# Kernel tuning notes

Measured on AMD Instinct MI355X. Metric: run time of the kernel, lower is better.

Reference implementation:

```python
import jax, jax.numpy as jnp
import numpy as np

T, B, D_IN, D_H, D_OUT, N_LAYERS = 512, 64, 512, 1024, 512, 2
LN_EPS = 1e-5


def _gru_layer(x_seq, h0, w_ih, w_hh, b_ih, b_hh):
    # x_seq: [T,B,D_in], h0: [B,H]; w_ih: [3H,D_in], w_hh: [3H,H]
    # Precompute input-side gate projections for all timesteps at once.
    xg = jnp.einsum('tbd,gd->tbg', x_seq, w_ih) + b_ih  # [T,B,3H]

    def step(h, xg_t):
        hg = h @ w_hh.T + b_hh                         # [B,3H]
        xr, xz, xn = jnp.split(xg_t, 3, axis=-1)
        hr, hz, hn = jnp.split(hg, 3, axis=-1)
        r = jax.nn.sigmoid(xr + hr)
        z = jax.nn.sigmoid(xz + hz)
        n = jnp.tanh(xn + r * hn)
        h_new = (1.0 - z) * n + z * h
        return h_new, h_new

    _, ys = jax.lax.scan(step, h0, xg)                 # ys: [T,B,H]
    return ys


def setup_inputs() -> dict:
    key = jax.random.key(0)
    ks = jax.random.split(key, 16)
    s_in = 1.0 / np.sqrt(D_H)
    inp = {
        'x': jax.random.normal(ks[0], (T, B, D_IN), dtype=jnp.float32),
        'h': jax.random.normal(ks[1], (N_LAYERS, B, D_H), dtype=jnp.float32),
        # GRU layer 0 (input dim D_IN)
        'w_ih0': jax.random.uniform(ks[2], (3 * D_H, D_IN), minval=-s_in, maxval=s_in),
        'w_hh0': jax.random.uniform(ks[3], (3 * D_H, D_H), minval=-s_in, maxval=s_in),
        'b_ih0': jax.random.uniform(ks[4], (3 * D_H,), minval=-s_in, maxval=s_in),
        'b_hh0': jax.random.uniform(ks[5], (3 * D_H,), minval=-s_in, maxval=s_in),
        # GRU layer 1 (input dim D_H)
        'w_ih1': jax.random.uniform(ks[6], (3 * D_H, D_H), minval=-s_in, maxval=s_in),
        'w_hh1': jax.random.uniform(ks[7], (3 * D_H, D_H), minval=-s_in, maxval=s_in),
        'b_ih1': jax.random.uniform(ks[8], (3 * D_H,), minval=-s_in, maxval=s_in),
        'b_hh1': jax.random.uniform(ks[9], (3 * D_H,), minval=-s_in, maxval=s_in),
        # LayerNorm
        'ln_gamma': jnp.ones((D_H,), dtype=jnp.float32),
        'ln_beta': jnp.zeros((D_H,), dtype=jnp.float32),
        # Output linear
        'ff_w': jax.random.uniform(ks[10], (D_OUT, D_H), minval=-s_in, maxval=s_in),
        'ff_b': jax.random.uniform(ks[11], (D_OUT,), minval=-s_in, maxval=s_in),
    }
    return inp


def reference(x, h, w_ih0, w_hh0, b_ih0, b_hh0, w_ih1, w_hh1, b_ih1, b_hh1,
              ln_gamma, ln_beta, ff_w, ff_b):
    y0 = _gru_layer(x, h[0], w_ih0, w_hh0, b_ih0, b_hh0)   # [T,B,H]
    y1 = _gru_layer(y0, h[1], w_ih1, w_hh1, b_ih1, b_hh1)  # [T,B,H]
    # LayerNorm over last dim
    mu = jnp.mean(y1, axis=-1, keepdims=True)
    var = jnp.mean(jnp.square(y1 - mu), axis=-1, keepdims=True)
    yn = (y1 - mu) * jax.lax.rsqrt(var + LN_EPS) * ln_gamma + ln_beta
    # Output projection
    out = jnp.einsum('tbh,oh->tbo', yn, ff_w) + ff_b       # [T,B,D_OUT]
    return out
```

## Files before the change

kernel.cpp:

```cpp
#include <hip/hip_runtime.h>

#define T_SEQ 512
#define BATCH 64
#define DIN0  512
#define D_H   1024
#define D_OUT 512
#define NBLK  256

typedef __attribute__((ext_vector_type(8))) short short8;
typedef __attribute__((ext_vector_type(4))) float f32x4;

__device__ inline float bf2f(unsigned short u) {
    unsigned x = ((unsigned)u) << 16;
    return __builtin_bit_cast(float, x);
}
__device__ inline unsigned short f2bf(float f) {
    unsigned x = __builtin_bit_cast(unsigned, f);
    unsigned r = (x + 0x7fffu + ((x >> 16) & 1u)) >> 16;
    return (unsigned short)r;
}
__device__ inline float fast_sigmoid(float x) { return 1.f / (1.f + __expf(-x)); }
__device__ inline float fast_tanh(float x) {
    float ax = fabsf(x);
    float t = __expf(-2.f * ax);
    float r = (1.f - t) / (1.f + t);
    return copysignf(r, x);
}

__device__ inline void store_u16_sc01(void* p, unsigned v) {
    asm volatile("global_store_short %0, %1, off sc0 sc1" :: "v"(p), "v"(v) : "memory");
}
__device__ inline void store_flag(int* p, int v) {
    asm volatile("global_store_dword %0, %1, off sc0 sc1" :: "v"(p), "v"(v) : "memory");
}
__device__ inline int load_flag(const int* p) {
    int r;
    asm volatile("global_load_dword %0, %1, off sc0 sc1\n\ts_waitcnt vmcnt(0)"
                 : "=&v"(r) : "v"(p) : "memory");
    return r;
}
__device__ inline short8 load16_sc01(const void* p) {
    short8 r;
    asm volatile("global_load_dwordx4 %0, %1, off sc0 sc1"
                 : "=&v"(r) : "v"(p) : "memory");
    return r;
}

__global__ void cast_kernel(const float* __restrict__ in, unsigned short* __restrict__ out, int n4) {
    int i = blockIdx.x * blockDim.x + threadIdx.x;
    int stride = gridDim.x * blockDim.x;
    for (; i < n4; i += stride) {
        float4 v = ((const float4*)in)[i];
        ushort4 o;
        o.x = f2bf(v.x); o.y = f2bf(v.y); o.z = f2bf(v.z); o.w = f2bf(v.w);
        ((ushort4*)out)[i] = o;
    }
}

template <int DIN, bool FULLZ>
__global__ __launch_bounds__(64, 1) void gru_scan(
    const unsigned short* __restrict__ xseq,
    const unsigned short* __restrict__ wih,
    const unsigned short* __restrict__ whh,
    const float* __restrict__ bih, const float* __restrict__ bhh,
    const float* __restrict__ h0,
    unsigned short* __restrict__ hbuf,
    unsigned short* __restrict__ Y,
    int* __restrict__ flags)
{
    extern __shared__ unsigned short lds[];
    constexpr int KT = D_H + DIN;

    const int lane = threadIdx.x;
    const int bid  = blockIdx.x;
    const int xcd = bid & 7;
    const int rg  = xcd >> 1;
    const int cb  = ((bid >> 3) << 1) | (xcd & 1);
    const int c0  = cb * 16, r0 = rg * 16;

    int* const frg   = flags + rg * 1024;
    int* const myflg = frg + cb * 16;

    const int NG = FULLZ ? 3 : 2;
    for (int g = 0; g < NG; ++g) {
        const int grow = (g == 0) ? 2 * D_H : (g == 1 ? 0 : D_H);
        unsigned short* W = lds + g * 16 * KT;
        for (int i = lane; i < 16 * (D_H / 8); i += 64) {
            int c = i >> 7, kb = i & 127;
            int el = (c * KT + kb * 8) ^ ((c & 7) << 3);
            *(short8*)&W[el] = *(const short8*)&whh[(size_t)(grow + c0 + c) * D_H + kb * 8];
        }
        for (int i = lane; i < 16 * (DIN / 8); i += 64) {
            int c = i / (DIN / 8), kb = i % (DIN / 8);
            int el = (c * KT + D_H + kb * 8) ^ ((c & 7) << 3);
            *(short8*)&W[el] = *(const short8*)&wih[(size_t)(grow + c0 + c) * DIN + kb * 8];
        }
    }
    if (!FULLZ) {
        for (int i = lane; i < 16 * (D_H / 8); i += 64) {
            int c = i >> 7, kb = i & 127;
            int el = 32 * KT + ((c * D_H + kb * 8) ^ ((c & 7) << 3));
            *(short8*)&lds[el] = *(const short8*)&whh[(size_t)(D_H + c0 + c) * D_H + kb * 8];
        }
    }
    __syncthreads();

    const int gc   = c0 + (lane & 15);
    const int crow = (lane >> 4) * 4;
    float hprev[4];
    #pragma unroll
    for (int i = 0; i < 4; ++i) {
        float v = h0[(size_t)(r0 + crow + i) * D_H + gc];
        hprev[i] = v;
        store_u16_sc01(&hbuf[(size_t)(r0 + crow + i) * D_H + gc], (unsigned)f2bf(v));
    }
    asm volatile("s_waitcnt vmcnt(0)" ::: "memory");
    if (lane == 0) store_flag(myflg, 1);

    const float b_r  = bih[gc] + bhh[gc];
    const float b_z  = bih[D_H + gc] + bhh[D_H + gc];
    const float b_xn = bih[2 * D_H + gc];
    const float b_hn = bhh[2 * D_H + gc];

    const int arow = lane & 15;
    const int ako  = (lane >> 4) * 8;
    const int swz  = (arow & 7) << 3;

    for (int t = 0; t < T_SEQ; ++t) {
        const unsigned short* hb  = hbuf + (t & 1) * (BATCH * D_H);
        unsigned short*       hbn = hbuf + ((t & 1) ^ 1) * (BATCH * D_H);
        const unsigned short* xt  = xseq + (size_t)t * BATCH * DIN;
        unsigned short*       Yt  = Y + (size_t)t * BATCH * D_H;

        f32x4 fr = {0.f, 0.f, 0.f, 0.f}, fz = fr, fnx = fr, fnh = fr;

        #pragma unroll 4
        for (int k = 0; k < DIN; k += 32) {
            short8 a  = *(const short8*)&xt[(size_t)(r0 + arow) * DIN + k + ako];
            int el    = (arow * KT + D_H + k + ako) ^ swz;
            short8 bn = *(const short8*)&lds[el];
            short8 br = *(const short8*)&lds[16 * KT + el];
            short8 bz;
            if (FULLZ) bz = *(const short8*)&lds[32 * KT + el];
            else       bz = *(const short8*)&wih[(size_t)(D_H + c0 + arow) * DIN + k + ako];
            fr  = __builtin_amdgcn_mfma_f32_16x16x32_bf16(a, br, fr, 0, 0, 0);
            fz  = __builtin_amdgcn_mfma_f32_16x16x32_bf16(a, bz, fz, 0, 0, 0);
            fnx = __builtin_amdgcn_mfma_f32_16x16x32_bf16(a, bn, fnx, 0, 0, 0);
        }

        {
            const int p = t + 1;
            const int* fp = frg + lane * 16;
            while (true) {
                int f = load_flag(fp);
                if (__all(f >= p)) break;
            }
        }

        short8 hfrag[32];
        const unsigned short* hrow = hb + (size_t)(r0 + arow) * D_H + ako;
        #pragma unroll
        for (int kk = 0; kk < 32; ++kk)
            hfrag[kk] = load16_sc01(hrow + kk * 32);
        asm volatile("s_waitcnt vmcnt(0)" ::: "memory");
        __builtin_amdgcn_sched_barrier(0);

        #pragma unroll
        for (int kk = 0; kk < 32; ++kk) {
            const int k = kk * 32;
            int el    = (arow * KT + k + ako) ^ swz;
            short8 bn = *(const short8*)&lds[el];
            short8 br = *(const short8*)&lds[16 * KT + el];
            int zel   = FULLZ ? (32 * KT + el)
                              : (32 * KT + ((arow * D_H + k + ako) ^ swz));
            short8 bz = *(const short8*)&lds[zel];
            fr  = __builtin_amdgcn_mfma_f32_16x16x32_bf16(hfrag[kk], br, fr, 0, 0, 0);
            fz  = __builtin_amdgcn_mfma_f32_16x16x32_bf16(hfrag[kk], bz, fz, 0, 0, 0);
            fnh = __builtin_amdgcn_mfma_f32_16x16x32_bf16(hfrag[kk], bn, fnh, 0, 0, 0);
        }

        #pragma unroll
        for (int i = 0; i < 4; ++i) {
            int rr = r0 + crow + i;
            float r = fast_sigmoid(fr[i] + b_r);
            float z = fast_sigmoid(fz[i] + b_z);
            float n = fast_tanh(fnx[i] + b_xn + r * (fnh[i] + b_hn));
            float hn = (1.f - z) * n + z * hprev[i];
            hprev[i] = hn;
            unsigned short h16 = f2bf(hn);
            store_u16_sc01(&hbn[(size_t)rr * D_H + gc], (unsigned)h16);
            Yt[(size_t)rr * D_H + gc] = h16;
        }
        asm volatile("s_waitcnt vmcnt(0)" ::: "memory");
        if (lane == 0) store_flag(myflg, t + 2);
    }
}

__global__ __launch_bounds__(256) void ln_proj(
    const unsigned short* __restrict__ y1,
    const float* __restrict__ gamma, const float* __restrict__ beta,
    const unsigned short* __restrict__ ffw,
    const float* __restrict__ ffb,
    float* __restrict__ out)
{
    __shared__ unsigned short ylds[16 * 1024];
    const int row0 = blockIdx.x * 16;
    const int tid = threadIdx.x;

    {
        const int rr = tid >> 4, l16 = tid & 15;
        const unsigned short* yrow = y1 + (size_t)(row0 + rr) * D_H;
        float s = 0.f, sq = 0.f;
        #pragma unroll
        for (int j8 = 0; j8 < 8; ++j8) {
            int k = l16 * 64 + j8 * 8;
            short8 v = *(const short8*)&yrow[k];
            int idx = (rr * 1024 + k) ^ ((rr & 7) << 3);
            *(short8*)&ylds[idx] = v;
            #pragma unroll
            for (int j = 0; j < 8; ++j) {
                float f = bf2f((unsigned short)v[j]);
                s += f; sq += f * f;
            }
        }
        #pragma unroll
        for (int o = 1; o < 16; o <<= 1) {
            s  += __shfl_xor(s, o, 64);
            sq += __shfl_xor(sq, o, 64);
        }
        float mu = s * (1.f / 1024.f);
        float var = sq * (1.f / 1024.f) - mu * mu;
        float rstd = rsqrtf(var + 1e-5f);
        #pragma unroll
        for (int j8 = 0; j8 < 8; ++j8) {
            int k = l16 * 64 + j8 * 8;
            int idx = (rr * 1024 + k) ^ ((rr & 7) << 3);
            short8 v = *(short8*)&ylds[idx];
            short8 o8;
            #pragma unroll
            for (int j = 0; j < 8; ++j) {
                float f = bf2f((unsigned short)v[j]);
                f = (f - mu) * rstd * gamma[k + j] + beta[k + j];
                o8[j] = (short)f2bf(f);
            }
            *(short8*)&ylds[idx] = o8;
        }
    }
    __syncthreads();

    const int w = tid >> 6, lane = tid & 63;
    const int cbase = w * 128;
    const int arow = lane & 15, ako = (lane >> 4) * 8;
    f32x4 acc[8] = {};
    for (int k = 0; k < D_H; k += 32) {
        int aidx = (arow * 1024 + k + ako) ^ ((arow & 7) << 3);
        short8 a = *(const short8*)&ylds[aidx];
        #pragma unroll
        for (int n = 0; n < 8; ++n) {
            int col = cbase + n * 16 + (lane & 15);
            short8 b = *(const short8*)&ffw[col * 1024 + k + ako];
            acc[n] = __builtin_amdgcn_mfma_f32_16x16x32_bf16(a, b, acc[n], 0, 0, 0);
        }
    }
    #pragma unroll
    for (int n = 0; n < 8; ++n) {
        int col = cbase + n * 16 + (lane & 15);
        float bb = ffb[col];
        #pragma unroll
        for (int i = 0; i < 4; ++i) {
            int rr = row0 + (lane >> 4) * 4 + i;
            out[(size_t)rr * D_OUT + col] = acc[n][i] + bb;
        }
    }
}

extern "C" void kernel_launch(void* const* d_in, const int* in_sizes, int n_in,
                              void* d_out, int out_size, void* d_ws, size_t ws_size,
                              hipStream_t stream) {
    const float* x     = (const float*)d_in[0];
    const float* h     = (const float*)d_in[1];
    const float* w_ih0 = (const float*)d_in[2];
    const float* w_hh0 = (const float*)d_in[3];
    const float* b_ih0 = (const float*)d_in[4];
    const float* b_hh0 = (const float*)d_in[5];
    const float* w_ih1 = (const float*)d_in[6];
    const float* w_hh1 = (const float*)d_in[7];
    const float* b_ih1 = (const float*)d_in[8];
    const float* b_hh1 = (const float*)d_in[9];
    const float* ln_g  = (const float*)d_in[10];
    const float* ln_b  = (const float*)d_in[11];
    const float* ff_w  = (const float*)d_in[12];
    const float* ff_b  = (const float*)d_in[13];
    float* out = (float*)d_out;

    char* ws = (char*)d_ws;
    size_t off = 0;
    auto alloc = [&](size_t bytes) {
        void* p = ws + off;
        off = (off + bytes + 255) & ~(size_t)255;
        return p;
    };
    unsigned short* x_bf   = (unsigned short*)alloc((size_t)T_SEQ * BATCH * DIN0 * 2);
    unsigned short* y1_bf  = (unsigned short*)alloc((size_t)T_SEQ * BATCH * D_H * 2);
    unsigned short* wih0_b = (unsigned short*)alloc((size_t)3 * D_H * DIN0 * 2);
    unsigned short* whh0_b = (unsigned short*)alloc((size_t)3 * D_H * D_H * 2);
    unsigned short* wih1_b = (unsigned short*)alloc((size_t)3 * D_H * D_H * 2);
    unsigned short* whh1_b = (unsigned short*)alloc((size_t)3 * D_H * D_H * 2);
    unsigned short* ffw_b  = (unsigned short*)alloc((size_t)D_OUT * D_H * 2);
    unsigned short* hbuf   = (unsigned short*)alloc((size_t)2 * BATCH * D_H * 2);
    int*            flags  = (int*)alloc(2 * 4096 * 4);
    if (off > ws_size) return;

    unsigned short* y0_bf = (unsigned short*)d_out;

    hipMemsetAsync(flags, 0, 2 * 4096 * 4, stream);

    auto castl = [&](const float* src, unsigned short* dst, int n) {
        int n4 = n / 4;
        int blocks = (n4 + 255) / 256;
        if (blocks > 2048) blocks = 2048;
        hipLaunchKernelGGL(cast_kernel, dim3(blocks), dim3(256), 0, stream, src, dst, n4);
    };
    castl(x,     x_bf,   T_SEQ * BATCH * DIN0);
    castl(w_ih0, wih0_b, 3 * D_H * DIN0);
    castl(w_hh0, whh0_b, 3 * D_H * D_H);
    castl(w_ih1, wih1_b, 3 * D_H * D_H);
    castl(w_hh1, whh1_b, 3 * D_H * D_H);
    castl(ff_w,  ffw_b,  D_OUT * D_H);

    const int lds0 = 48 * (D_H + DIN0) * 2;
    const int lds1 = 32 * (D_H + D_H) * 2 + 16 * D_H * 2;
    hipFuncSetAttribute((const void*)&gru_scan<DIN0, true>,
                        hipFuncAttributeMaxDynamicSharedMemorySize, lds0);
    hipFuncSetAttribute((const void*)&gru_scan<D_H, false>,
                        hipFuncAttributeMaxDynamicSharedMemorySize, lds1);

    hipLaunchKernelGGL((gru_scan<DIN0, true>), dim3(NBLK), dim3(64), lds0, stream,
        x_bf, wih0_b, whh0_b, b_ih0, b_hh0, h, hbuf, y0_bf, flags);
    hipLaunchKernelGGL((gru_scan<D_H, false>), dim3(NBLK), dim3(64), lds1, stream,
        y0_bf, wih1_b, whh1_b, b_ih1, b_hh1, h + BATCH * D_H, hbuf, y1_bf,
        flags + 4096);
    hipLaunchKernelGGL(ln_proj, dim3(T_SEQ * BATCH / 16), dim3(256), 0, stream,
        y1_bf, ln_g, ln_b, ffw_b, ff_b, out);
}
```

Baseline: 8.312 ms.

## Tile hidden-state buffer and chunk flag waits to overlap recurrent matmul with sync

Changes the hidden-state exchange buffer to a tiled 16x16 layout and packs per-block progress flags as 16-bit values so one 16-byte load checks eight producers. The recurrent matmul is split into eight chunks, each waiting only on the eight blocks that produce that slice of h, so MFMA work can start before all 64 producers finish. The Y store moves after the flag publish, and the spin loop gains s_sleep and an iteration cap. The cap risks silently proceeding with stale data on a timeout, and the many small waits add latency.

```diff
diff --git a/kernel.cpp b/kernel.cpp
--- a/kernel.cpp
+++ b/kernel.cpp
@@ -6,6 +6,7 @@
 #define D_H   1024
 #define D_OUT 512
 #define NBLK  256
+#define TILES 65536
 
 typedef __attribute__((ext_vector_type(8))) short short8;
 typedef __attribute__((ext_vector_type(4))) float f32x4;
@@ -30,21 +31,20 @@
 __device__ inline void store_u16_sc01(void* p, unsigned v) {
     asm volatile("global_store_short %0, %1, off sc0 sc1" :: "v"(p), "v"(v) : "memory");
 }
-__device__ inline void store_flag(int* p, int v) {
-    asm volatile("global_store_dword %0, %1, off sc0 sc1" :: "v"(p), "v"(v) : "memory");
-}
-__device__ inline int load_flag(const int* p) {
-    int r;
-    asm volatile("global_load_dword %0, %1, off sc0 sc1\n\ts_waitcnt vmcnt(0)"
-                 : "=&v"(r) : "v"(p) : "memory");
-    return r;
-}
 __device__ inline short8 load16_sc01(const void* p) {
     short8 r;
     asm volatile("global_load_dwordx4 %0, %1, off sc0 sc1"
                  : "=&v"(r) : "v"(p) : "memory");
     return r;
 }
+__device__ inline short8 load16_sc01_wait(const void* p) {
+    short8 r;
+    asm volatile("global_load_dwordx4 %0, %1, off sc0 sc1\n\ts_waitcnt vmcnt(0)"
+                 : "=&v"(r) : "v"(p) : "memory");
+    return r;
+}
+
+#define MFMA16(a, b, c) __builtin_amdgcn_mfma_f32_16x16x32_bf16((a), (b), (c), 0, 0, 0)
 
 __global__ void cast_kernel(const float* __restrict__ in, unsigned short* __restrict__ out, int n4) {
     int i = blockIdx.x * blockDim.x + threadIdx.x;
@@ -66,133 +66,141 @@
     const float* __restrict__ h0,
     unsigned short* __restrict__ hbuf,
     unsigned short* __restrict__ Y,
-    int* __restrict__ flags)
+    unsigned short* __restrict__ flags)
 {
     extern __shared__ unsigned short lds[];
-    constexpr int KT = D_H + DIN;
+    constexpr int KT = 1024 + DIN;
 
     const int lane = threadIdx.x;
     const int bid  = blockIdx.x;
-    const int xcd = bid & 7;
-    const int rg  = xcd >> 1;
-    const int cb  = ((bid >> 3) << 1) | (xcd & 1);
-    const int c0  = cb * 16, r0 = rg * 16;
-
-    int* const frg   = flags + rg * 1024;
-    int* const myflg = frg + cb * 16;
+    const int xcd  = bid & 7;
+    const int rg   = xcd >> 1;
+    const int cb   = ((bid >> 3) << 1) | (xcd & 1);
+    const int c0   = cb * 16, r0 = rg * 16;
+    const int tile = rg * 64 + cb;
+
+    unsigned short* const frg   = flags + rg * 64;
+    unsigned short* const myflg = frg + cb;
 
     const int NG = FULLZ ? 3 : 2;
     for (int g = 0; g < NG; ++g) {
         const int grow = (g == 0) ? 2 * D_H : (g == 1 ? 0 : D_H);
         unsigned short* W = lds + g * 16 * KT;
-        for (int i = lane; i < 16 * (D_H / 8); i += 64) {
+        for (int i = lane; i < 16 * 128; i += 64) {
             int c = i >> 7, kb = i & 127;
             int el = (c * KT + kb * 8) ^ ((c & 7) << 3);
             *(short8*)&W[el] = *(const short8*)&whh[(size_t)(grow + c0 + c) * D_H + kb * 8];
         }
         for (int i = lane; i < 16 * (DIN / 8); i += 64) {
             int c = i / (DIN / 8), kb = i % (DIN / 8);
-            int el = (c * KT + D_H + kb * 8) ^ ((c & 7) << 3);
+            int el = (c * KT + 1024 + kb * 8) ^ ((c & 7) << 3);
             *(short8*)&W[el] = *(const short8*)&wih[(size_t)(grow + c0 + c) * DIN + kb * 8];
         }
     }
     if (!FULLZ) {
-        for (int i = lane; i < 16 * (D_H / 8); i += 64) {
+        for (int i = lane; i < 16 * 128; i += 64) {
             int c = i >> 7, kb = i & 127;
-            int el = 32 * KT + ((c * D_H + kb * 8) ^ ((c & 7) << 3));
+            int el = 32 * KT + ((c * 1024 + kb * 8) ^ ((c & 7) << 3));
             *(short8*)&lds[el] = *(const short8*)&whh[(size_t)(D_H + c0 + c) * D_H + kb * 8];
         }
     }
-    __syncthreads();
-
-    const int gc   = c0 + (lane & 15);
+
+    const int arow = lane & 15;
+    const int ako  = (lane >> 4) * 8;
+    const int swz  = (arow & 7) << 3;
+    const int gc   = c0 + arow;
     const int crow = (lane >> 4) * 4;
+
+    const float b_r  = bih[gc] + bhh[gc];
+    const float b_z  = bih[D_H + gc] + bhh[D_H + gc];
+    const float b_xn = bih[2 * D_H + gc];
+    const float b_hn = bhh[2 * D_H + gc];
+
     float hprev[4];
     #pragma unroll
     for (int i = 0; i < 4; ++i) {
         float v = h0[(size_t)(r0 + crow + i) * D_H + gc];
         hprev[i] = v;
-        store_u16_sc01(&hbuf[(size_t)(r0 + crow + i) * D_H + gc], (unsigned)f2bf(v));
+        store_u16_sc01(&hbuf[tile * 256 + (crow + i) * 16 + arow], (unsigned)f2bf(v));
     }
     asm volatile("s_waitcnt vmcnt(0)" ::: "memory");
-    if (lane == 0) store_flag(myflg, 1);
-
-    const float b_r  = bih[gc] + bhh[gc];
-    const float b_z  = bih[D_H + gc] + bhh[D_H + gc];
-    const float b_xn = bih[2 * D_H + gc];
-    const float b_hn = bhh[2 * D_H + gc];
-
-    const int arow = lane & 15;
-    const int ako  = (lane >> 4) * 8;
-    const int swz  = (arow & 7) << 3;
+    if (lane == 0) store_u16_sc01(myflg, 1u);
 
     for (int t = 0; t < T_SEQ; ++t) {
-        const unsigned short* hb  = hbuf + (t & 1) * (BATCH * D_H);
-        unsigned short*       hbn = hbuf + ((t & 1) ^ 1) * (BATCH * D_H);
+        const unsigned short* hb  = hbuf + (t & 1) * TILES;
+        unsigned short*       hbn = hbuf + ((t & 1) ^ 1) * TILES;
         const unsigned short* xt  = xseq + (size_t)t * BATCH * DIN;
         unsigned short*       Yt  = Y + (size_t)t * BATCH * D_H;
 
-        f32x4 fr = {0.f, 0.f, 0.f, 0.f}, fz = fr, fnx = fr, fnh = fr;
+        f32x4 fr = {0.f,0.f,0.f,0.f}, fz = fr, fnx = fr, fnh = fr;
 
         #pragma unroll 4
         for (int k = 0; k < DIN; k += 32) {
             short8 a  = *(const short8*)&xt[(size_t)(r0 + arow) * DIN + k + ako];
-            int el    = (arow * KT + D_H + k + ako) ^ swz;
+            int el    = (arow * KT + 1024 + k + ako) ^ swz;
             short8 bn = *(const short8*)&lds[el];
             short8 br = *(const short8*)&lds[16 * KT + el];
             short8 bz;
             if (FULLZ) bz = *(const short8*)&lds[32 * KT + el];
             else       bz = *(const short8*)&wih[(size_t)(D_H + c0 + arow) * DIN + k + ako];
-            fr  = __builtin_amdgcn_mfma_f32_16x16x32_bf16(a, br, fr, 0, 0, 0);
-            fz  = __builtin_amdgcn_mfma_f32_16x16x32_bf16(a, bz, fz, 0, 0, 0);
-            fnx = __builtin_amdgcn_mfma_f32_16x16x32_bf16(a, bn, fnx, 0, 0, 0);
-        }
-
-        {
-            const int p = t + 1;
-            const int* fp = frg + lane * 16;
-            while (true) {
-                int f = load_flag(fp);
-                if (__all(f >= p)) break;
-            }
-        }
-
-        short8 hfrag[32];
-        const unsigned short* hrow = hb + (size_t)(r0 + arow) * D_H + ako;
-        #pragma unroll
-        for (int kk = 0; kk < 32; ++kk)
-            hfrag[kk] = load16_sc01(hrow + kk * 32);
-        asm volatile("s_waitcnt vmcnt(0)" ::: "memory");
-        __builtin_amdgcn_sched_barrier(0);
-
-        #pragma unroll
-        for (int kk = 0; kk < 32; ++kk) {
-            const int k = kk * 32;
-            int el    = (arow * KT + k + ako) ^ swz;
-            short8 bn = *(const short8*)&lds[el];
-            short8 br = *(const short8*)&lds[16 * KT + el];
-            int zel   = FULLZ ? (32 * KT + el)
-                              : (32 * KT + ((arow * D_H + k + ako) ^ swz));
-            short8 bz = *(const short8*)&lds[zel];
-            fr  = __builtin_amdgcn_mfma_f32_16x16x32_bf16(hfrag[kk], br, fr, 0, 0, 0);
-            fz  = __builtin_amdgcn_mfma_f32_16x16x32_bf16(hfrag[kk], bz, fz, 0, 0, 0);
-            fnh = __builtin_amdgcn_mfma_f32_16x16x32_bf16(hfrag[kk], bn, fnh, 0, 0, 0);
-        }
-
+            fnx = MFMA16(a, bn, fnx);
+            fr  = MFMA16(a, br, fr);
+            fz  = MFMA16(a, bz, fz);
+        }
+
+        for (int c = 0; c < 8; ++c) {
+            const int ch = (c + (cb & 7)) & 7;
+            {
+                const unsigned short* fp = frg + ch * 8;
+                for (int it = 0; it < 100000; ++it) {
+                    short8 f = load16_sc01_wait(fp);
+                    bool ok = true;
+                    #pragma unroll
+                    for (int j = 0; j < 8; ++j)
+                        ok &= ((unsigned short)f[j] >= (unsigned)(t + 1));
+                    if (__all(ok)) break;
+                    __builtin_amdgcn_s_sleep(1);
+                }
+            }
+            short8 hf[4];
+            #pragma unroll
+            for (int m = 0; m < 4; ++m) {
+                int tk = rg * 64 + ch * 8 + m * 2 + (ako >> 4);
+                hf[m] = load16_sc01(hb + (size_t)tk * 256 + arow * 16 + (ako & 8));
+            }
+            asm volatile("s_waitcnt vmcnt(0)" ::: "memory");
+            __builtin_amdgcn_sched_barrier(0);
+            #pragma unroll
+            for (int m = 0; m < 4; ++m) {
+                const int k = ch * 128 + m * 32;
+                int el    = (arow * KT + k + ako) ^ swz;
+                short8 bn = *(const short8*)&lds[el];
+                short8 br = *(const short8*)&lds[16 * KT + el];
+                short8 bz;
+                if (FULLZ) bz = *(const short8*)&lds[32 * KT + el];
+                else       bz = *(const short8*)&lds[32 * KT + ((arow * 1024 + k + ako) ^ swz)];
+                fnh = MFMA16(hf[m], bn, fnh);
+                fr  = MFMA16(hf[m], br, fr);
+                fz  = MFMA16(hf[m], bz, fz);
+            }
+        }
+
+        unsigned short h16[4];
         #pragma unroll
         for (int i = 0; i < 4; ++i) {
-            int rr = r0 + crow + i;
             float r = fast_sigmoid(fr[i] + b_r);
             float z = fast_sigmoid(fz[i] + b_z);
             float n = fast_tanh(fnx[i] + b_xn + r * (fnh[i] + b_hn));
             float hn = (1.f - z) * n + z * hprev[i];
             hprev[i] = hn;
-            unsigned short h16 = f2bf(hn);
-            store_u16_sc01(&hbn[(size_t)rr * D_H + gc], (unsigned)h16);
-            Yt[(size_t)rr * D_H + gc] = h16;
+            h16[i] = f2bf(hn);
+            store_u16_sc01(&hbn[tile * 256 + (crow + i) * 16 + arow], (unsigned)h16[i]);
         }
         asm volatile("s_waitcnt vmcnt(0)" ::: "memory");
-        if (lane == 0) store_flag(myflg, t + 2);
+        if (lane == 0) store_u16_sc01(myflg, (unsigned)(t + 2));
+        #pragma unroll
+        for (int i = 0; i < 4; ++i)
+            Yt[(size_t)(r0 + crow + i) * D_H + gc] = h16[i];
     }
 }
 
@@ -307,13 +315,13 @@
     unsigned short* wih1_b = (unsigned short*)alloc((size_t)3 * D_H * D_H * 2);
     unsigned short* whh1_b = (unsigned short*)alloc((size_t)3 * D_H * D_H * 2);
     unsigned short* ffw_b  = (unsigned short*)alloc((size_t)D_OUT * D_H * 2);
-    unsigned short* hbuf   = (unsigned short*)alloc((size_t)2 * BATCH * D_H * 2);
-    int*            flags  = (int*)alloc(2 * 4096 * 4);
+    unsigned short* hbuf   = (unsigned short*)alloc((size_t)2 * TILES * 2);
+    unsigned short* flags  = (unsigned short*)alloc(2 * 4 * 64 * 2);
     if (off > ws_size) return;
 
     unsigned short* y0_bf = (unsigned short*)d_out;
 
-    hipMemsetAsync(flags, 0, 2 * 4096 * 4, stream);
+    hipMemsetAsync(flags, 0, 2 * 4 * 64 * 2, stream);
 
     auto castl = [&](const float* src, unsigned short* dst, int n) {
         int n4 = n / 4;
@@ -328,8 +336,8 @@
     castl(w_hh1, whh1_b, 3 * D_H * D_H);
     castl(ff_w,  ffw_b,  D_OUT * D_H);
 
-    const int lds0 = 48 * (D_H + DIN0) * 2;
-    const int lds1 = 32 * (D_H + D_H) * 2 + 16 * D_H * 2;
+    const int lds0 = 3 * 16 * (1024 + DIN0) * 2;
+    const int lds1 = (2 * 16 * (1024 + D_H) + 16 * 1024) * 2;
     hipFuncSetAttribute((const void*)&gru_scan<DIN0, true>,
                         hipFuncAttributeMaxDynamicSharedMemorySize, lds0);
     hipFuncSetAttribute((const void*)&gru_scan<D_H, false>,
@@ -339,7 +347,7 @@
         x_bf, wih0_b, whh0_b, b_ih0, b_hh0, h, hbuf, y0_bf, flags);
     hipLaunchKernelGGL((gru_scan<D_H, false>), dim3(NBLK), dim3(64), lds1, stream,
         y0_bf, wih1_b, whh1_b, b_ih1, b_hh1, h + BATCH * D_H, hbuf, y1_bf,
-        flags + 4096);
+        flags + 256);
     hipLaunchKernelGGL(ln_proj, dim3(T_SEQ * BATCH / 16), dim3(256), 0, stream,
         y1_bf, ln_g, ln_b, ffw_b, ff_b, out);
 }
```

Result: slower. 9.741 ms (+17.2%).
